# Optimization experiments

Measured on AMD Instinct MI355X. Metric: run time of the kernel, lower is better.

Reference implementation:

```python
import jax, jax.numpy as jnp
import numpy as np

BETA = 0.25
NUM_EMBEDDINGS = 512
DIM_EMBEDDING = 64


def setup_inputs() -> dict:
    key = jax.random.key(0)
    k1, k2 = jax.random.split(key)
    z_e = jax.random.normal(k1, (32, 64, 64, 64), dtype=jnp.float32)
    # torch init: uniform_(-1/num_embeddings, 1/num_embeddings)
    lim = 1.0 / NUM_EMBEDDINGS
    embeddings = jax.random.uniform(
        k2, (NUM_EMBEDDINGS, DIM_EMBEDDING), dtype=jnp.float32,
        minval=-lim, maxval=lim)
    return {"z_e": z_e, "embeddings": embeddings}


def reference(z_e, embeddings):
    # Flatten exactly as torch's z_e.view(-1, dim_embedding) on (N,C,H,W)
    z_flat = z_e.reshape(-1, DIM_EMBEDDING)          # [M, D]
    # Squared euclidean distances: ||z||^2 + ||e||^2 - 2 z e^T
    distances = (
        jnp.sum(z_flat ** 2, axis=1, keepdims=True)
        + jnp.sum(embeddings ** 2, axis=1)
        - 2.0 * jnp.matmul(z_flat, embeddings.T)
    )                                                # [M, K]
    encoding_indices = jnp.argmin(distances, axis=1)[:, None]  # [M, 1]
    quantized = embeddings[encoding_indices[:, 0]].reshape(z_e.shape)
    # Straight-through estimator
    quantized_st = z_e + jax.lax.stop_gradient(quantized - z_e)
    recon_loss = jnp.mean((jax.lax.stop_gradient(quantized_st) - z_e) ** 2)
    commitment_loss = BETA * jnp.mean(
        (quantized_st - jax.lax.stop_gradient(z_e)) ** 2)
    loss = recon_loss + commitment_loss
    return (loss, quantized_st, encoding_indices)
```

## Files before the change

### kernel.cpp

```cpp
#include <hip/hip_runtime.h>
#include <hip/hip_bf16.h>

constexpr int NELEM = 8388608;
constexpr int ROWS  = 64;
constexpr int NBLK  = 131072 / ROWS;
constexpr int ZS    = 68;
constexpr float EPS = 1e-3f;
constexpr int QCAP  = 1024;

typedef short bf16x8 __attribute__((ext_vector_type(8)));
typedef float v4f    __attribute__((ext_vector_type(4)));

__device__ bf16x8 g_efrag[32][2][64];
__device__ float  g_en2[512];

__device__ inline bf16x8 cvt_hi8(const float* __restrict__ s, float scale) {
    bf16x8 h;
#pragma unroll
    for (int j = 0; j < 8; ++j) {
        __hip_bfloat16 b = __float2bfloat16(scale * s[j]);
        h[j] = (short)__bfloat16_as_ushort(b);
    }
    return h;
}

__global__ void __launch_bounds__(256) vq_prep(const float* __restrict__ emb,
                                               float* __restrict__ out) {
    const int b = blockIdx.x;
    if (b < 16) {
        const int id   = b * 256 + threadIdx.x;
        const int lane = id & 63;
        const int kc   = (id >> 6) & 1;
        const int ct   = id >> 7;
        const float* src = emb + (size_t)(ct * 16 + (lane & 15)) * 64
                               + kc * 32 + (lane >> 4) * 8;
        g_efrag[ct][kc][lane] = cvt_hi8(src, -2.0f);
    } else {
#pragma unroll
        for (int c = 0; c < 2; ++c) {
            const int k = threadIdx.x + c * 256;
            const float4* e4 = (const float4*)(emb + (size_t)k * 64);
            float a = 0.f, bq = 0.f, cc = 0.f, d = 0.f;
#pragma unroll
            for (int i = 0; i < 16; ++i) {
                float4 v = e4[i];
                a += v.x * v.x; bq += v.y * v.y; cc += v.z * v.z; d += v.w * v.w;
            }
            g_en2[k] = (a + bq) + (cc + d);
        }
        if (threadIdx.x == 0) out[0] = 0.f;
    }
}

__global__ __launch_bounds__(256) __attribute__((amdgpu_waves_per_eu(4, 4)))
void vq_main(const float* __restrict__ z,
             const float* __restrict__ emb,
             float* __restrict__ out) {
    __shared__ float s_z[ROWS * ZS];
    __shared__ float s_en2[512];
    __shared__ float s_zn2[ROWS];
    __shared__ unsigned long long s_key[ROWS];
    __shared__ float s_wmin[ROWS][4];
    __shared__ float s_thr[ROWS];
    __shared__ unsigned s_q[QCAP];
    __shared__ int s_qn;
    __shared__ float s_lpart[4];

    const int tid  = threadIdx.x;
    const int lane = tid & 63;
    const int wid  = __builtin_amdgcn_readfirstlane(tid >> 6);
    const int mcol = lane & 15;
    const int quad = lane >> 4;

    {
        const int row = tid >> 2, seg = tid & 3;
        const float4* gp = (const float4*)(z + ((size_t)blockIdx.x * ROWS + row) * 64 + seg * 16);
#pragma unroll
        for (int i = 0; i < 4; ++i)
            *(float4*)&s_z[row * ZS + seg * 16 + i * 4] = gp[i];
    }
    s_en2[tid]       = g_en2[tid];
    s_en2[tid + 256] = g_en2[tid + 256];
    if (tid < ROWS) s_key[tid] = ~0ULL;
    if (tid == 0) s_qn = 0;
    __syncthreads();

    {
        const int row = tid >> 2, s = tid & 3;
        const float* zr = &s_z[row * ZS];
        float p = 0.f;
#pragma unroll
        for (int i = 0; i < 16; ++i) p += zr[4 * i + s] * zr[4 * i + s];
        p += __shfl_xor(p, 1, 64);
        p += __shfl_xor(p, 2, 64);
        if (s == 0) s_zn2[row] = p;
    }

    bf16x8 zf[4][2];
#pragma unroll
    for (int rg = 0; rg < 4; ++rg) {
        zf[rg][0] = cvt_hi8(&s_z[(rg * 16 + mcol) * ZS +  0 + quad * 8], 1.0f);
        zf[rg][1] = cvt_hi8(&s_z[(rg * 16 + mcol) * ZS + 32 + quad * 8], 1.0f);
    }

    float lmin[4];
#pragma unroll
    for (int rg = 0; rg < 4; ++rg) lmin[rg] = 3.402823466e38f;
#pragma unroll
    for (int ct = 0; ct < 8; ++ct) {
        const int gct = wid * 8 + ct;
        bf16x8 e0 = g_efrag[gct][0][lane];
        bf16x8 e1 = g_efrag[gct][1][lane];
        v4f base = *(const v4f*)&s_en2[gct * 16 + quad * 4];
#pragma unroll
        for (int rg = 0; rg < 4; ++rg) {
            v4f a = base;
            a = __builtin_amdgcn_mfma_f32_16x16x32_bf16(e0, zf[rg][0], a, 0, 0, 0);
            a = __builtin_amdgcn_mfma_f32_16x16x32_bf16(e1, zf[rg][1], a, 0, 0, 0);
            lmin[rg] = fminf(lmin[rg], fminf(fminf(a.x, a.y), fminf(a.z, a.w)));
        }
    }

#pragma unroll
    for (int rg = 0; rg < 4; ++rg) {
        float m = lmin[rg];
        m = fminf(m, __shfl_xor(m, 16, 64));
        m = fminf(m, __shfl_xor(m, 32, 64));
        if (quad == 0) s_wmin[rg * 16 + mcol][wid] = m;
    }
    __syncthreads();
    if (tid < ROWS)
        s_thr[tid] = fminf(fminf(s_wmin[tid][0], s_wmin[tid][1]),
                           fminf(s_wmin[tid][2], s_wmin[tid][3])) + EPS;
    __syncthreads();

    float thr[4];
#pragma unroll
    for (int rg = 0; rg < 4; ++rg) thr[rg] = s_thr[rg * 16 + mcol];
#pragma unroll
    for (int ct = 0; ct < 8; ++ct) {
        const int gct = wid * 8 + ct;
        bf16x8 e0 = g_efrag[gct][0][lane];
        bf16x8 e1 = g_efrag[gct][1][lane];
        v4f base = *(const v4f*)&s_en2[gct * 16 + quad * 4];
#pragma unroll
        for (int rg = 0; rg < 4; ++rg) {
            v4f a = base;
            a = __builtin_amdgcn_mfma_f32_16x16x32_bf16(e0, zf[rg][0], a, 0, 0, 0);
            a = __builtin_amdgcn_mfma_f32_16x16x32_bf16(e1, zf[rg][1], a, 0, 0, 0);
            float m4 = fminf(fminf(a.x, a.y), fminf(a.z, a.w));
            if (m4 <= thr[rg]) {
#pragma unroll
                for (int r = 0; r < 4; ++r) {
                    if (a[r] <= thr[rg]) {
                        int slot = atomicAdd(&s_qn, 1);
                        if (slot < QCAP)
                            s_q[slot] = ((unsigned)(rg * 16 + mcol) << 16) |
                                        (unsigned)(wid * 128 + ct * 16 + quad * 4 + r);
                    }
                }
            }
        }
    }
    __syncthreads();

    {
        const int qn = s_qn;
        for (int i = tid; i < qn && i < QCAP; i += 256) {
            const unsigned e = s_q[i];
            const int row = e >> 16, code = e & 0xFFFF;
            const float* zr = &s_z[row * ZS];
            const float* er = emb + (size_t)code * 64;
            float a = 0.f, b = 0.f, c2 = 0.f, d = 0.f;
#pragma unroll
            for (int g = 0; g < 16; ++g) {
                a  += zr[4*g]   * er[4*g];   b += zr[4*g+1] * er[4*g+1];
                c2 += zr[4*g+2] * er[4*g+2]; d += zr[4*g+3] * er[4*g+3];
            }
            float dot  = (a + b) + (c2 + d);
            float dist = (s_zn2[row] + s_en2[code]) - 2.0f * dot;
            unsigned long long key =
                ((unsigned long long)__float_as_uint(dist) << 32) | (unsigned)code;
            atomicMin(&s_key[row], key);
        }
    }
    __syncthreads();

    const int row = tid >> 2, seg = tid & 3;
    const int widx = (int)(unsigned)(s_key[row] & 0x1FFULL);
    const float* er = emb + (size_t)widx * 64 + seg * 16;
    const float* zr = &s_z[row * ZS + seg * 16];
    float* qo = out + 1 + ((size_t)blockIdx.x * ROWS + row) * 64 + seg * 16;
    float lsum = 0.f;
#pragma unroll
    for (int j = 0; j < 16; ++j) {
        float zv = zr[j], ev = er[j];
        float q = zv + (ev - zv);
        float df = q - zv; lsum += df * df;
        qo[j] = q;
    }
    if (seg == 0)
        out[1 + NELEM + blockIdx.x * ROWS + row] = (float)widx;

#pragma unroll
    for (int off = 32; off; off >>= 1) lsum += __shfl_down(lsum, off, 64);
    if (lane == 0) s_lpart[wid] = lsum;
    __syncthreads();
    if (tid == 0) {
        float p = (s_lpart[0] + s_lpart[1]) + (s_lpart[2] + s_lpart[3]);
        atomicAdd(out, p * (1.25f / 8388608.0f));
    }
}

extern "C" void kernel_launch(void* const* d_in, const int* in_sizes, int n_in,
                              void* d_out, int out_size, void* d_ws, size_t ws_size,
                              hipStream_t stream) {
    const float* z   = (const float*)d_in[0];
    const float* emb = (const float*)d_in[1];
    float* out = (float*)d_out;

    vq_prep<<<17, 256, 0, stream>>>(emb, out);
    vq_main<<<NBLK, 256, 0, stream>>>(z, emb, out);
}
```

Before: 159.9 us.

## Split work by rows per wave instead of codebook slices, drop cross-wave min sync

Each wave now owns 16 rows and scans the full 512-entry codebook, rather than each wave scanning a quarter of the codebook for all 64 rows. The per-row min is then reduced inside the wave with shuffles, which removes the shared-memory min table and two block barriers. In exchange each wave reads all 32 codebook fragments from global memory (four times more fragment loads per wave), and there is less independent MFMA work per fragment load for latency hiding.

```diff
diff --git a/kernel.cpp b/kernel.cpp
--- a/kernel.cpp
+++ b/kernel.cpp
@@ -60,8 +60,6 @@
     __shared__ float s_en2[512];
     __shared__ float s_zn2[ROWS];
     __shared__ unsigned long long s_key[ROWS];
-    __shared__ float s_wmin[ROWS][4];
-    __shared__ float s_thr[ROWS];
     __shared__ unsigned s_q[QCAP];
     __shared__ int s_qn;
     __shared__ float s_lpart[4];
@@ -96,68 +94,40 @@
         if (s == 0) s_zn2[row] = p;
     }
 
-    bf16x8 zf[4][2];
+    const int zrow = wid * 16 + mcol;
+    const bf16x8 zf0 = cvt_hi8(&s_z[zrow * ZS +  0 + quad * 8], 1.0f);
+    const bf16x8 zf1 = cvt_hi8(&s_z[zrow * ZS + 32 + quad * 8], 1.0f);
+
+    float lmin = 3.402823466e38f;
 #pragma unroll
-    for (int rg = 0; rg < 4; ++rg) {
-        zf[rg][0] = cvt_hi8(&s_z[(rg * 16 + mcol) * ZS +  0 + quad * 8], 1.0f);
-        zf[rg][1] = cvt_hi8(&s_z[(rg * 16 + mcol) * ZS + 32 + quad * 8], 1.0f);
+    for (int ct = 0; ct < 32; ++ct) {
+        bf16x8 e0 = g_efrag[ct][0][lane];
+        bf16x8 e1 = g_efrag[ct][1][lane];
+        v4f a = *(const v4f*)&s_en2[ct * 16 + quad * 4];
+        a = __builtin_amdgcn_mfma_f32_16x16x32_bf16(e0, zf0, a, 0, 0, 0);
+        a = __builtin_amdgcn_mfma_f32_16x16x32_bf16(e1, zf1, a, 0, 0, 0);
+        lmin = fminf(lmin, fminf(fminf(a.x, a.y), fminf(a.z, a.w)));
     }
-
-    float lmin[4];
-#pragma unroll
-    for (int rg = 0; rg < 4; ++rg) lmin[rg] = 3.402823466e38f;
-#pragma unroll
-    for (int ct = 0; ct < 8; ++ct) {
-        const int gct = wid * 8 + ct;
-        bf16x8 e0 = g_efrag[gct][0][lane];
-        bf16x8 e1 = g_efrag[gct][1][lane];
-        v4f base = *(const v4f*)&s_en2[gct * 16 + quad * 4];
-#pragma unroll
-        for (int rg = 0; rg < 4; ++rg) {
-            v4f a = base;
-            a = __builtin_amdgcn_mfma_f32_16x16x32_bf16(e0, zf[rg][0], a, 0, 0, 0);
-            a = __builtin_amdgcn_mfma_f32_16x16x32_bf16(e1, zf[rg][1], a, 0, 0, 0);
-            lmin[rg] = fminf(lmin[rg], fminf(fminf(a.x, a.y), fminf(a.z, a.w)));
-        }
-    }
+    lmin = fminf(lmin, __shfl_xor(lmin, 16, 64));
+    lmin = fminf(lmin, __shfl_xor(lmin, 32, 64));
+    const float thr = lmin + EPS;
 
 #pragma unroll
-    for (int rg = 0; rg < 4; ++rg) {
-        float m = lmin[rg];
-        m = fminf(m, __shfl_xor(m, 16, 64));
-        m = fminf(m, __shfl_xor(m, 32, 64));
-        if (quad == 0) s_wmin[rg * 16 + mcol][wid] = m;
-    }
-    __syncthreads();
-    if (tid < ROWS)
-        s_thr[tid] = fminf(fminf(s_wmin[tid][0], s_wmin[tid][1]),
-                           fminf(s_wmin[tid][2], s_wmin[tid][3])) + EPS;
-    __syncthreads();
-
-    float thr[4];
+    for (int ct = 0; ct < 32; ++ct) {
+        bf16x8 e0 = g_efrag[ct][0][lane];
+        bf16x8 e1 = g_efrag[ct][1][lane];
+        v4f a = *(const v4f*)&s_en2[ct * 16 + quad * 4];
+        a = __builtin_amdgcn_mfma_f32_16x16x32_bf16(e0, zf0, a, 0, 0, 0);
+        a = __builtin_amdgcn_mfma_f32_16x16x32_bf16(e1, zf1, a, 0, 0, 0);
+        float m4 = fminf(fminf(a.x, a.y), fminf(a.z, a.w));
+        if (m4 <= thr) {
 #pragma unroll
-    for (int rg = 0; rg < 4; ++rg) thr[rg] = s_thr[rg * 16 + mcol];
-#pragma unroll
-    for (int ct = 0; ct < 8; ++ct) {
-        const int gct = wid * 8 + ct;
-        bf16x8 e0 = g_efrag[gct][0][lane];
-        bf16x8 e1 = g_efrag[gct][1][lane];
-        v4f base = *(const v4f*)&s_en2[gct * 16 + quad * 4];
-#pragma unroll
-        for (int rg = 0; rg < 4; ++rg) {
-            v4f a = base;
-            a = __builtin_amdgcn_mfma_f32_16x16x32_bf16(e0, zf[rg][0], a, 0, 0, 0);
-            a = __builtin_amdgcn_mfma_f32_16x16x32_bf16(e1, zf[rg][1], a, 0, 0, 0);
-            float m4 = fminf(fminf(a.x, a.y), fminf(a.z, a.w));
-            if (m4 <= thr[rg]) {
-#pragma unroll
-                for (int r = 0; r < 4; ++r) {
-                    if (a[r] <= thr[rg]) {
-                        int slot = atomicAdd(&s_qn, 1);
-                        if (slot < QCAP)
-                            s_q[slot] = ((unsigned)(rg * 16 + mcol) << 16) |
-                                        (unsigned)(wid * 128 + ct * 16 + quad * 4 + r);
-                    }
+            for (int r = 0; r < 4; ++r) {
+                if (a[r] <= thr) {
+                    int slot = atomicAdd(&s_qn, 1);
+                    if (slot < QCAP)
+                        s_q[slot] = ((unsigned)zrow << 16) |
+                                    (unsigned)(ct * 16 + quad * 4 + r);
                 }
             }
         }
```

After: 172.6 us. 1.08x slower.
